# Performance work log

Hardware: AMD Instinct MI355X
Metric: run time of the kernel (lower is better)

## Reference

```python
import jax, jax.numpy as jnp
import numpy as np
import math

D_MODEL = 1024
N_HEADS = 16
D_K = D_MODEL // N_HEADS


def setup_inputs() -> dict:
    key = jax.random.key(0)
    ks = jax.random.split(key, 9)
    B, N = 2, 8192
    s = 1.0 / math.sqrt(D_MODEL)
    x = jax.random.normal(ks[0], (B, N, D_MODEL), dtype=jnp.float32)
    Wq = jax.random.normal(ks[1], (D_MODEL, D_MODEL), dtype=jnp.float32) * s
    bq = jnp.zeros((D_MODEL,), dtype=jnp.float32)
    Wk = jax.random.normal(ks[2], (D_MODEL, D_MODEL), dtype=jnp.float32) * s
    bk = jnp.zeros((D_MODEL,), dtype=jnp.float32)
    Wv = jax.random.normal(ks[3], (D_MODEL, D_MODEL), dtype=jnp.float32) * s
    bv = jnp.zeros((D_MODEL,), dtype=jnp.float32)
    Wo = jax.random.normal(ks[4], (D_MODEL, D_MODEL), dtype=jnp.float32) * s
    bo = jnp.zeros((D_MODEL,), dtype=jnp.float32)
    return {"x": x, "Wq": Wq, "bq": bq, "Wk": Wk, "bk": bk,
            "Wv": Wv, "bv": bv, "Wo": Wo, "bo": bo}


def _fft_circulant_attention(Q, K, V):
    # Q,K,V: (B,H,N,d_k); FFT along the sequence axis (axis=2)
    B, H, N, d_k = Q.shape
    scale = 1.0 / math.sqrt(d_k)
    Q_fft = jnp.fft.rfft(Q, axis=2)
    K_fft = jnp.fft.rfft(K, axis=2)
    # circular cross-correlation summed over d_k -> (B,H,Nf)
    scores_fft = jnp.sum(Q_fft * jnp.conj(K_fft), axis=-1)
    scores = jnp.fft.irfft(scores_fft, n=N, axis=2) * scale  # (B,H,N)
    attn = jax.nn.softmax(scores, axis=-1)                    # (B,H,N)
    attn_fft = jnp.fft.rfft(attn, axis=2)                     # (B,H,Nf)
    V_fft = jnp.fft.rfft(V, axis=2)                           # (B,H,Nf,d_k)
    out_fft = attn_fft[..., None] * V_fft
    return jnp.fft.irfft(out_fft, n=N, axis=2)                # (B,H,N,d_k)


def reference(x, Wq, bq, Wk, bk, Wv, bv, Wo, bo):
    B, N, _ = x.shape
    # torch Linear: x @ W.T + b
    def proj(W, b):
        return (x @ W.T + b).reshape(B, N, N_HEADS, D_K).transpose(0, 2, 1, 3)
    Q = proj(Wq, bq)
    K = proj(Wk, bk)
    V = proj(Wv, bv)
    O = _fft_circulant_attention(Q, K, V)          # (B,H,N,d_k)
    O = O.transpose(0, 2, 1, 3).reshape(B, N, D_MODEL)
    return O @ Wo.T + bo
```

## Files before the change

kernel.cpp:

```cpp
#include <hip/hip_runtime.h>
#include <math.h>
#include <stdint.h>

#define NDIM 8192
#define DM 1024
#define NH 16
#define DKH 64
#define BATCH 2
#define NSPLIT 16
#define NTF 256
#define NPTF (NDIM / NTF)

typedef __attribute__((ext_vector_type(8))) short short8v;
typedef __attribute__((ext_vector_type(4))) float f32x4;

__device__ inline float bf2f(unsigned short u) {
  return __uint_as_float(((unsigned int)u) << 16);
}
__device__ inline unsigned short f2bf(float f) {
  unsigned int u = __float_as_uint(f);
  u += 0x7fffu + ((u >> 16) & 1u);
  return (unsigned short)(u >> 16);
}
__device__ inline float2 cmul(float2 a, float2 b) {
  return make_float2(a.x * b.x - a.y * b.y, a.x * b.y + a.y * b.x);
}
__device__ inline float2 cmulc(float2 a, float2 b) {
  return make_float2(a.x * b.x + a.y * b.y, a.y * b.x - a.x * b.y);
}

__device__ inline void gload_lds16(const void* g, void* l) {
  __builtin_amdgcn_global_load_lds(
      (const __attribute__((address_space(1))) unsigned int*)(uintptr_t)g,
      (__attribute__((address_space(3))) unsigned int*)(uintptr_t)l, 16, 0, 0);
}

__global__ void twiddle_init(float2* tw) {
  int k = blockIdx.x * blockDim.x + threadIdx.x;
  if (k < NDIM) {
    double a = -2.0 * 3.14159265358979323846 * (double)k / (double)NDIM;
    tw[k] = make_float2((float)cos(a), (float)sin(a));
  }
}

__global__ __launch_bounds__(256)
void split_x(const float* __restrict__ x, unsigned short* __restrict__ xhi,
             unsigned short* __restrict__ xlo) {
  size_t i = ((size_t)blockIdx.x * 256 + threadIdx.x) * 4;
  float4 v = *(const float4*)&x[i];
  ushort4 h, l;
  h.x = f2bf(v.x); l.x = f2bf(v.x - bf2f(h.x));
  h.y = f2bf(v.y); l.y = f2bf(v.y - bf2f(h.y));
  h.z = f2bf(v.z); l.z = f2bf(v.z - bf2f(h.z));
  h.w = f2bf(v.w); l.w = f2bf(v.w - bf2f(h.w));
  *(ushort4*)&xhi[i] = h;
  *(ushort4*)&xlo[i] = l;
}

__global__ __launch_bounds__(256)
void split_w(const float* __restrict__ Wq, const float* __restrict__ Wk,
             const float* __restrict__ Wv, const float* __restrict__ Wo,
             unsigned short* __restrict__ whi, unsigned short* __restrict__ wlo,
             unsigned short* __restrict__ wob) {
  int z = blockIdx.z;
  const float* W = (z == 0) ? Wq : ((z == 1) ? Wk : ((z == 2) ? Wv : Wo));
  size_t i = ((size_t)blockIdx.x * 256 + threadIdx.x) * 4;
  float4 v = *(const float4*)&W[i];
  ushort4 h, l;
  h.x = f2bf(v.x); l.x = f2bf(v.x - bf2f(h.x));
  h.y = f2bf(v.y); l.y = f2bf(v.y - bf2f(h.y));
  h.z = f2bf(v.z); l.z = f2bf(v.z - bf2f(h.z));
  h.w = f2bf(v.w); l.w = f2bf(v.w - bf2f(h.w));
  if (z < 3) {
    *(ushort4*)&whi[(size_t)z * DM * DM + i] = h;
    *(ushort4*)&wlo[(size_t)z * DM * DM + i] = l;
  } else {
    *(ushort4*)&wob[i] = h;
  }
}

__device__ inline void fft_fwd(float2* __restrict__ s, const float2* __restrict__ tw, int tid) {
  const float C = 0.70710678118654752f;
  for (int lm = 10; lm >= 1; lm -= 3) {
    int m = 1 << lm;
    int sh = 10 - lm;
    __syncthreads();
    for (int t = tid; t < NDIM / 8; t += NTF) {
      int p = t & (m - 1);
      int i0 = ((t >> lm) << (lm + 3)) + p;
      float2 x0 = s[i0],       x1 = s[i0 + m],     x2 = s[i0 + 2 * m], x3 = s[i0 + 3 * m];
      float2 x4 = s[i0 + 4 * m], x5 = s[i0 + 5 * m], x6 = s[i0 + 6 * m], x7 = s[i0 + 7 * m];
      float2 e0 = {x0.x + x4.x, x0.y + x4.y}, o0 = {x0.x - x4.x, x0.y - x4.y};
      float2 e1 = {x1.x + x5.x, x1.y + x5.y}, o1 = {x1.x - x5.x, x1.y - x5.y};
      float2 e2 = {x2.x + x6.x, x2.y + x6.y}, o2 = {x2.x - x6.x, x2.y - x6.y};
      float2 e3 = {x3.x + x7.x, x3.y + x7.y}, o3 = {x3.x - x7.x, x3.y - x7.y};
      float2 t1 = {C * (o1.x + o1.y), C * (o1.y - o1.x)};
      float2 t2 = {o2.y, -o2.x};
      float2 t3 = {C * (o3.y - o3.x), -C * (o3.x + o3.y)};
      float2 pe = {e0.x + e2.x, e0.y + e2.y}, qe = {e0.x - e2.x, e0.y - e2.y};
      float2 re = {e1.x + e3.x, e1.y + e3.y}, se = {e1.x - e3.x, e1.y - e3.y};
      float2 po = {o0.x + t2.x, o0.y + t2.y}, qo = {o0.x - t2.x, o0.y - t2.y};
      float2 ro = {t1.x + t3.x, t1.y + t3.y}, so = {t1.x - t3.x, t1.y - t3.y};
      float2 y0 = {pe.x + re.x, pe.y + re.y};
      float2 y4 = {pe.x - re.x, pe.y - re.y};
      float2 y2 = {qe.x + se.y, qe.y - se.x};
      float2 y6 = {qe.x - se.y, qe.y + se.x};
      float2 y1 = {po.x + ro.x, po.y + ro.y};
      float2 y5 = {po.x - ro.x, po.y - ro.y};
      float2 y3 = {qo.x + so.y, qo.y - so.x};
      float2 y7 = {qo.x - so.y, qo.y + so.x};
      int e = p << sh;
      s[i0]         = y0;
      s[i0 + m]     = cmul(y1, tw[e]);
      s[i0 + 2 * m] = cmul(y2, tw[2 * e]);
      s[i0 + 3 * m] = cmul(y3, tw[3 * e]);
      s[i0 + 4 * m] = cmul(y4, tw[4 * e]);
      s[i0 + 5 * m] = cmul(y5, tw[5 * e]);
      s[i0 + 6 * m] = cmul(y6, tw[6 * e]);
      s[i0 + 7 * m] = cmul(y7, tw[7 * e]);
    }
  }
  __syncthreads();
  for (int t = tid; t < NDIM / 2; t += NTF) {
    int i0 = t * 2;
    float2 u = s[i0], v = s[i0 + 1];
    s[i0]     = make_float2(u.x + v.x, u.y + v.y);
    s[i0 + 1] = make_float2(u.x - v.x, u.y - v.y);
  }
  __syncthreads();
}

__device__ inline void fft_inv(float2* __restrict__ s, const float2* __restrict__ tw, int tid) {
  const float C = 0.70710678118654752f;
  __syncthreads();
  for (int t = tid; t < NDIM / 2; t += NTF) {
    int i0 = t * 2;
    float2 u = s[i0], v = s[i0 + 1];
    s[i0]     = make_float2(u.x + v.x, u.y + v.y);
    s[i0 + 1] = make_float2(u.x - v.x, u.y - v.y);
  }
  for (int lm = 1; lm <= 10; lm += 3) {
    int m = 1 << lm;
    int sh = 10 - lm;
    __syncthreads();
    for (int t = tid; t < NDIM / 8; t += NTF) {
      int p = t & (m - 1);
      int i0 = ((t >> lm) << (lm + 3)) + p;
      int e = p << sh;
      float2 z0 = s[i0];
      float2 z1 = cmulc(s[i0 + m],     tw[e]);
      float2 z2 = cmulc(s[i0 + 2 * m], tw[2 * e]);
      float2 z3 = cmulc(s[i0 + 3 * m], tw[3 * e]);
      float2 z4 = cmulc(s[i0 + 4 * m], tw[4 * e]);
      float2 z5 = cmulc(s[i0 + 5 * m], tw[5 * e]);
      float2 z6 = cmulc(s[i0 + 6 * m], tw[6 * e]);
      float2 z7 = cmulc(s[i0 + 7 * m], tw[7 * e]);
      float2 E0 = {z0.x + z4.x, z0.y + z4.y}, O0 = {z0.x - z4.x, z0.y - z4.y};
      float2 E1 = {z1.x + z5.x, z1.y + z5.y}, O1 = {z1.x - z5.x, z1.y - z5.y};
      float2 E2 = {z2.x + z6.x, z2.y + z6.y}, O2 = {z2.x - z6.x, z2.y - z6.y};
      float2 E3 = {z3.x + z7.x, z3.y + z7.y}, O3 = {z3.x - z7.x, z3.y - z7.y};
      float2 T1 = {C * (O1.x - O1.y), C * (O1.x + O1.y)};
      float2 T2 = {-O2.y, O2.x};
      float2 T3 = {-C * (O3.x + O3.y), C * (O3.x - O3.y)};
      float2 PE = {E0.x + E2.x, E0.y + E2.y}, QE = {E0.x - E2.x, E0.y - E2.y};
      float2 RE = {E1.x + E3.x, E1.y + E3.y}, SE = {E1.x - E3.x, E1.y - E3.y};
      float2 PO = {O0.x + T2.x, O0.y + T2.y}, QO = {O0.x - T2.x, O0.y - T2.y};
      float2 RO = {T1.x + T3.x, T1.y + T3.y}, SO = {T1.x - T3.x, T1.y - T3.y};
      s[i0]         = make_float2(PE.x + RE.x, PE.y + RE.y);
      s[i0 + 4 * m] = make_float2(PE.x - RE.x, PE.y - RE.y);
      s[i0 + 2 * m] = make_float2(QE.x - SE.y, QE.y + SE.x);
      s[i0 + 6 * m] = make_float2(QE.x + SE.y, QE.y - SE.x);
      s[i0 + m]     = make_float2(PO.x + RO.x, PO.y + RO.y);
      s[i0 + 5 * m] = make_float2(PO.x - RO.x, PO.y - RO.y);
      s[i0 + 3 * m] = make_float2(QO.x - SO.y, QO.y + SO.x);
      s[i0 + 7 * m] = make_float2(QO.x + SO.y, QO.y - SO.x);
    }
  }
  __syncthreads();
}

__device__ inline float blk_max(float v, float* red, int tid) {
  #pragma unroll
  for (int o = 32; o > 0; o >>= 1) v = fmaxf(v, __shfl_down(v, o, 64));
  __syncthreads();
  if ((tid & 63) == 0) red[tid >> 6] = v;
  __syncthreads();
  float r = fmaxf(fmaxf(red[0], red[1]), fmaxf(red[2], red[3]));
  __syncthreads();
  return r;
}
__device__ inline float blk_sum(float v, float* red, int tid) {
  #pragma unroll
  for (int o = 32; o > 0; o >>= 1) v += __shfl_down(v, o, 64);
  __syncthreads();
  if ((tid & 63) == 0) red[tid >> 6] = v;
  __syncthreads();
  float r = (red[0] + red[1]) + (red[2] + red[3]);
  __syncthreads();
  return r;
}

__global__ __launch_bounds__(512, 4)
void proj_gemm_mfma(const unsigned short* __restrict__ xhi, const unsigned short* __restrict__ xlo,
                    const unsigned short* __restrict__ whi, const unsigned short* __restrict__ wlo,
                    const float* __restrict__ bq, const float* __restrict__ bk,
                    const float* __restrict__ bv,
                    float* __restrict__ Qt, float* __restrict__ Kt, unsigned short* __restrict__ Vt) {
  int raw = blockIdx.x;
  int swz = (raw & 7) * 384 + (raw >> 3);
  int nb = (swz & 63) * 128;
  int cb = ((swz >> 6) & 7) * 128;
  int z  = swz >> 9;
  int b = z / 3, wsel = z % 3;
  bool full = (wsel < 2);
  const unsigned short* Wh = whi + (size_t)wsel * DM * DM;
  const unsigned short* Wl = wlo + (size_t)wsel * DM * DM;
  const float* bias = (wsel == 0) ? bq : ((wsel == 1) ? bk : bv);
  __shared__ unsigned short lAh[128 * 64], lAl[128 * 64];
  __shared__ unsigned short lBh[128 * 64], lBl[128 * 64];
  int tid = threadIdx.x;
  int lane = tid & 63, wid = tid >> 6;
  int wr = wid >> 2, wc = wid & 3;
  int srow = tid >> 3, sg = tid & 7;
  const unsigned short* gAh = Wh + (size_t)cb * DM;
  const unsigned short* gAl = Wl + (size_t)cb * DM;
  const unsigned short* gBh = xhi + ((size_t)b * NDIM + nb) * DM;
  const unsigned short* gBl = xlo + ((size_t)b * NDIM + nb) * DM;

  f32x4 acc[4][2];
  #pragma unroll
  for (int i = 0; i < 4; ++i)
    #pragma unroll
    for (int j = 0; j < 2; ++j) acc[i][j] = (f32x4){0.f, 0.f, 0.f, 0.f};

  int col = lane & 15, kg = lane >> 4;
  for (int k0 = 0; k0 < DM; k0 += 64) {
    #pragma unroll
    for (int i = 0; i < 2; ++i) {
      int r = i * 64 + srow;
      int gc = (sg ^ (r & 7)) * 8;
      size_t go = (size_t)r * DM + k0 + gc;
      int lo_ = r * 64 + sg * 8;
      gload_lds16(gAh + go, &lAh[lo_]);
      gload_lds16(gBh + go, &lBh[lo_]);
      if (full) {
        gload_lds16(gAl + go, &lAl[lo_]);
        gload_lds16(gBl + go, &lBl[lo_]);
      }
    }
    asm volatile("s_waitcnt vmcnt(0)");
    __syncthreads();
    #pragma unroll
    for (int kk = 0; kk < 2; ++kk) {
      short8v ah[4], al[4], bh_[2], bl_[2];
      #pragma unroll
      for (int mi = 0; mi < 4; ++mi) {
        int r = wr * 64 + mi * 16 + col;
        int s = r * 64 + (((kk * 4 + kg) ^ (r & 7)) * 8);
        ah[mi] = *(const short8v*)&lAh[s];
        if (full) al[mi] = *(const short8v*)&lAl[s];
      }
      #pragma unroll
      for (int ni = 0; ni < 2; ++ni) {
        int r = wc * 32 + ni * 16 + col;
        int s = r * 64 + (((kk * 4 + kg) ^ (r & 7)) * 8);
        bh_[ni] = *(const short8v*)&lBh[s];
        if (full) bl_[ni] = *(const short8v*)&lBl[s];
      }
      #pragma unroll
      for (int mi = 0; mi < 4; ++mi)
        #pragma unroll
        for (int ni = 0; ni < 2; ++ni) {
          acc[mi][ni] = __builtin_amdgcn_mfma_f32_16x16x32_bf16(ah[mi], bh_[ni], acc[mi][ni], 0, 0, 0);
          if (full) {
            acc[mi][ni] = __builtin_amdgcn_mfma_f32_16x16x32_bf16(ah[mi], bl_[ni], acc[mi][ni], 0, 0, 0);
            acc[mi][ni] = __builtin_amdgcn_mfma_f32_16x16x32_bf16(al[mi], bh_[ni], acc[mi][ni], 0, 0, 0);
          }
        }
    }
    __syncthreads();
  }
  size_t obase = (size_t)b * DM * NDIM;
  #pragma unroll
  for (int mi = 0; mi < 4; ++mi) {
    #pragma unroll
    for (int reg = 0; reg < 4; ++reg) {
      int c = cb + wr * 64 + mi * 16 + kg * 4 + reg;
      float bsv = bias[c];
      #pragma unroll
      for (int ni = 0; ni < 2; ++ni) {
        int n = nb + wc * 32 + ni * 16 + col;
        float v = acc[mi][ni][reg] + bsv;
        if (wsel < 2) {
          float* out = ((wsel == 0) ? Qt : Kt) + obase;
          out[(size_t)c * NDIM + n] = v;
        } else {
          Vt[obase + (size_t)c * NDIM + n] = f2bf(v);
        }
      }
    }
  }
}

__global__ __launch_bounds__(256)
void score_fft_kernel(const float* __restrict__ Qt, const float* __restrict__ Kt,
                      const float2* __restrict__ tw, float2* __restrict__ part) {
  extern __shared__ float2 buf[];
  int bh = blockIdx.x / NSPLIT;
  int split = blockIdx.x % NSPLIT;
  int b = bh / NH, h = bh % NH;
  int tid = threadIdx.x;
  float qfx[NPTF], qfy[NPTF], accx[NPTF], accy[NPTF];
  #pragma unroll
  for (int i = 0; i < NPTF; ++i) { accx[i] = 0.f; accy[i] = 0.f; }

  for (int dp = 0; dp < 2; ++dp) {
    int c0 = h * DKH + (split * 2 + dp) * 2;
    const float* q0 = Qt + ((size_t)b * DM + c0) * NDIM;
    const float* q1 = q0 + NDIM;
    const float* k0c = Kt + ((size_t)b * DM + c0) * NDIM;
    const float* k1c = k0c + NDIM;
    #pragma unroll
    for (int i = 0; i < NPTF; ++i) {
      int ii = i * NTF + tid;
      buf[ii] = make_float2(q0[ii], q1[ii]);
    }
    fft_fwd(buf, tw, tid);
    #pragma unroll
    for (int i = 0; i < NPTF; ++i) { float2 v = buf[i * NTF + tid]; qfx[i] = v.x; qfy[i] = v.y; }
    #pragma unroll
    for (int i = 0; i < NPTF; ++i) {
      int ii = i * NTF + tid;
      buf[ii] = make_float2(k0c[ii], k1c[ii]);
    }
    fft_fwd(buf, tw, tid);
    #pragma unroll
    for (int i = 0; i < NPTF; ++i) {
      float2 kf = buf[i * NTF + tid];
      accx[i] += qfx[i] * kf.x + qfy[i] * kf.y;
      accy[i] += qfy[i] * kf.x - qfx[i] * kf.y;
    }
  }
  float2* dst = part + ((size_t)bh * NSPLIT + split) * NDIM;
  #pragma unroll
  for (int i = 0; i < NPTF; ++i) dst[i * NTF + tid] = make_float2(accx[i], accy[i]);
}

__global__ __launch_bounds__(256)
void reduce_part(const float2* __restrict__ part, float2* __restrict__ sred) {
  #pragma unroll
  for (int rep = 0; rep < 2; ++rep) {
    size_t g = (size_t)blockIdx.x * 512 + rep * 256 + threadIdx.x;
    int bh = (int)(g >> 13);
    int i  = (int)(g & (NDIM - 1));
    float sx = 0.f, sy = 0.f;
    #pragma unroll
    for (int s = 0; s < NSPLIT; ++s) {
      float2 v = part[((size_t)bh * NSPLIT + s) * NDIM + i];
      sx += v.x; sy += v.y;
    }
    sred[g] = make_float2(sx, sy);
  }
}

__global__ __launch_bounds__(256)
void softmax_attn_kernel(const float2* __restrict__ sred, const float2* __restrict__ tw,
                         float2* __restrict__ attnf) {
  extern __shared__ float2 buf[];
  int bh = blockIdx.x;
  int tid = threadIdx.x;
  for (int i = tid; i < NDIM; i += NTF) buf[i] = sred[(size_t)bh * NDIM + i];
  fft_inv(buf, tw, tid);
  const float scale = 0.125f / (float)NDIM;
  float vals[NPTF];
  float lmax = -3.0e38f;
  #pragma unroll
  for (int i = 0; i < NPTF; ++i) {
    float v = buf[i * NTF + tid].x * scale;
    vals[i] = v;
    lmax = fmaxf(lmax, v);
  }
  float* red = (float*)buf;
  float gmax = blk_max(lmax, red, tid);
  float lsum = 0.f;
  #pragma unroll
  for (int i = 0; i < NPTF; ++i) { float e = expf(vals[i] - gmax); vals[i] = e; lsum += e; }
  float gsum = blk_sum(lsum, red, tid);
  float inv = 1.0f / gsum;
  #pragma unroll
  for (int i = 0; i < NPTF; ++i) buf[i * NTF + tid] = make_float2(vals[i] * inv, 0.f);
  fft_fwd(buf, tw, tid);
  for (int i = tid; i < NDIM; i += NTF) attnf[(size_t)bh * NDIM + i] = buf[i];
}

__global__ __launch_bounds__(256)
void out_fft_kernel(const unsigned short* __restrict__ Vt, const float2* __restrict__ attnf,
                    const float2* __restrict__ tw, unsigned short* __restrict__ Ot) {
  extern __shared__ float2 buf[];
  int idx = blockIdx.x;
  int b = idx / (DM / 2), cp = idx % (DM / 2);
  int c0 = cp * 2;
  int h = c0 >> 6;
  int bh = b * NH + h;
  int tid = threadIdx.x;
  const unsigned short* v0 = Vt + ((size_t)b * DM + c0) * NDIM;
  const unsigned short* v1 = v0 + NDIM;
  for (int i = tid; i < NDIM; i += NTF) buf[i] = make_float2(bf2f(v0[i]), bf2f(v1[i]));
  fft_fwd(buf, tw, tid);
  for (int i = tid; i < NDIM; i += NTF) {
    float2 vf = buf[i];
    float2 af = attnf[(size_t)bh * NDIM + i];
    buf[i] = cmul(vf, af);
  }
  fft_inv(buf, tw, tid);
  const float invn = 1.0f / (float)NDIM;
  unsigned short* o0 = Ot + ((size_t)b * DM + c0) * NDIM;
  unsigned short* o1 = o0 + NDIM;
  for (int i = tid; i < NDIM; i += NTF) {
    float2 v = buf[i];
    o0[i] = f2bf(v.x * invn);
    o1[i] = f2bf(v.y * invn);
  }
}

__global__ __launch_bounds__(256)
void transpose_ot(const unsigned short* __restrict__ Ot, unsigned short* __restrict__ Ont) {
  int b = blockIdx.z;
  int cb = blockIdx.y * 64, n0 = blockIdx.x * 64;
  __shared__ unsigned short t[64][68];
  int tid = threadIdx.x;
  int r = tid >> 4, c4 = (tid & 15) * 4;
  const unsigned short* src = Ot + (size_t)b * DM * NDIM;
  #pragma unroll
  for (int i = 0; i < 4; ++i) {
    ushort4 v = *(const ushort4*)&src[(size_t)(cb + i * 16 + r) * NDIM + n0 + c4];
    *(ushort4*)&t[i * 16 + r][c4] = v;
  }
  __syncthreads();
  unsigned short* dst = Ont + (size_t)b * NDIM * DM;
  #pragma unroll
  for (int i = 0; i < 4; ++i) {
    int n = i * 16 + r;
    ushort4 v;
    v.x = t[c4 + 0][n]; v.y = t[c4 + 1][n]; v.z = t[c4 + 2][n]; v.w = t[c4 + 3][n];
    *(ushort4*)&dst[(size_t)(n0 + n) * DM + cb + c4] = v;
  }
}

__global__ __launch_bounds__(512, 4)
void final_gemm_mfma(const unsigned short* __restrict__ Ont, const unsigned short* __restrict__ Wob,
                     const float* __restrict__ bo, float* __restrict__ out) {
  int raw = blockIdx.x;
  int swz = (raw & 7) * 128 + (raw >> 3);
  int nb = (swz & 63) * 128;
  int pb = ((swz >> 6) & 7) * 128;
  int b  = swz >> 9;
  __shared__ unsigned short lA[128 * 64], lB[128 * 64];
  int tid = threadIdx.x;
  int lane = tid & 63, wid = tid >> 6;
  int wr = wid >> 2, wc = wid & 3;
  int srow = tid >> 3, sg = tid & 7;
  const unsigned short* gA = Ont + ((size_t)b * NDIM + nb) * DM;
  const unsigned short* gB = Wob + (size_t)pb * DM;

  f32x4 acc[4][2];
  #pragma unroll
  for (int i = 0; i < 4; ++i)
    #pragma unroll
    for (int j = 0; j < 2; ++j) acc[i][j] = (f32x4){0.f, 0.f, 0.f, 0.f};

  int col = lane & 15, kg = lane >> 4;
  for (int k0 = 0; k0 < DM; k0 += 64) {
    #pragma unroll
    for (int i = 0; i < 2; ++i) {
      int r = i * 64 + srow;
      int gc = (sg ^ (r & 7)) * 8;
      size_t go = (size_t)r * DM + k0 + gc;
      int lo_ = r * 64 + sg * 8;
      gload_lds16(gA + go, &lA[lo_]);
      gload_lds16(gB + go, &lB[lo_]);
    }
    asm volatile("s_waitcnt vmcnt(0)");
    __syncthreads();
    #pragma unroll
    for (int kk = 0; kk < 2; ++kk) {
      short8v af[4], bf[2];
      #pragma unroll
      for (int mi = 0; mi < 4; ++mi) {
        int r = wr * 64 + mi * 16 + col;
        af[mi] = *(const short8v*)&lA[r * 64 + (((kk * 4 + kg) ^ (r & 7)) * 8)];
      }
      #pragma unroll
      for (int ni = 0; ni < 2; ++ni) {
        int r = wc * 32 + ni * 16 + col;
        bf[ni] = *(const short8v*)&lB[r * 64 + (((kk * 4 + kg) ^ (r & 7)) * 8)];
      }
      #pragma unroll
      for (int mi = 0; mi < 4; ++mi)
        #pragma unroll
        for (int ni = 0; ni < 2; ++ni)
          acc[mi][ni] = __builtin_amdgcn_mfma_f32_16x16x32_bf16(af[mi], bf[ni], acc[mi][ni], 0, 0, 0);
    }
    __syncthreads();
  }
  #pragma unroll
  for (int mi = 0; mi < 4; ++mi) {
    #pragma unroll
    for (int reg = 0; reg < 4; ++reg) {
      int n = nb + wr * 64 + mi * 16 + kg * 4 + reg;
      size_t rowoff = ((size_t)b * NDIM + n) * DM;
      #pragma unroll
      for (int ni = 0; ni < 2; ++ni) {
        int cp = pb + wc * 32 + ni * 16 + col;
        out[rowoff + cp] = acc[mi][ni][reg] + bo[cp];
      }
    }
  }
}

extern "C" void kernel_launch(void* const* d_in, const int* in_sizes, int n_in,
                              void* d_out, int out_size, void* d_ws, size_t ws_size,
                              hipStream_t stream) {
  (void)in_sizes; (void)n_in; (void)out_size;
  const float* x  = (const float*)d_in[0];
  const float* Wq = (const float*)d_in[1]; const float* bq = (const float*)d_in[2];
  const float* Wk = (const float*)d_in[3]; const float* bk = (const float*)d_in[4];
  const float* Wv = (const float*)d_in[5]; const float* bv = (const float*)d_in[6];
  const float* Wo = (const float*)d_in[7]; const float* bo = (const float*)d_in[8];

  char* ws = (char*)d_ws;
  size_t off = 0;
  float2* tw = (float2*)(ws + off); off += (size_t)NDIM * sizeof(float2);
  float*  Qt = (float*)(ws + off);  off += (size_t)BATCH * DM * NDIM * 4;
  float*  Kt = (float*)(ws + off);  off += (size_t)BATCH * DM * NDIM * 4;
  unsigned short* Vt  = (unsigned short*)(ws + off); off += (size_t)BATCH * DM * NDIM * 2;
  size_t xhi_off = off;
  unsigned short* Xhi = (unsigned short*)(ws + off); off += (size_t)BATCH * NDIM * DM * 2;
  size_t xlo_off = off;
  unsigned short* Xlo = (unsigned short*)(ws + off); off += (size_t)BATCH * NDIM * DM * 2;
  unsigned short* Whi = (unsigned short*)(ws + off); off += (size_t)3 * DM * DM * 2;
  unsigned short* Wlo = (unsigned short*)(ws + off); off += (size_t)3 * DM * DM * 2;
  unsigned short* Wob = (unsigned short*)(ws + off); off += (size_t)DM * DM * 2;
  float2* part  = (float2*)(ws + xhi_off);
  float2* attnf = (float2*)(ws + xlo_off);
  float2* sred  = (float2*)(ws + xlo_off + 4194304);
  unsigned short* Ot  = (unsigned short*)Qt;
  unsigned short* Ont = (unsigned short*)Kt;

  if (ws_size < off) return;

  twiddle_init<<<32, 256, 0, stream>>>(tw);
  split_x<<<(BATCH * NDIM * DM) / (256 * 4), 256, 0, stream>>>(x, Xhi, Xlo);
  split_w<<<dim3((DM * DM) / (256 * 4), 1, 4), 256, 0, stream>>>(Wq, Wk, Wv, Wo, Whi, Wlo, Wob);

  proj_gemm_mfma<<<3072, 512, 0, stream>>>(Xhi, Xlo, Whi, Wlo, bq, bk, bv, Qt, Kt, Vt);

  score_fft_kernel<<<BATCH * NH * NSPLIT, NTF, NDIM * sizeof(float2), stream>>>(Qt, Kt, tw, part);
  reduce_part<<<(BATCH * NH * NDIM) / 512, 256, 0, stream>>>(part, sred);
  softmax_attn_kernel<<<BATCH * NH, NTF, NDIM * sizeof(float2), stream>>>(sred, tw, attnf);
  out_fft_kernel<<<BATCH * DM / 2, NTF, NDIM * sizeof(float2), stream>>>(Vt, attnf, tw, Ot);

  transpose_ot<<<dim3(NDIM / 64, DM / 64, BATCH), 256, 0, stream>>>(Ot, Ont);
  final_gemm_mfma<<<1024, 512, 0, stream>>>(Ont, Wob, bo, (float*)d_out);
}
```

Before: 571.3 us.

## Halve projection GEMM K-tile, raise occupancy bound, drop block swizzle

The projection GEMM now stages 32-wide K slices instead of 64, which halves its LDS footprint (from 64KB to 32KB) and changes the XOR swizzle to match the new row width. Both GEMMs raise the launch-bounds occupancy hint from 4 to 8 blocks per SM and replace the 1D swizzled block mapping with a plain 3D grid. The aim is more resident waves to hide load latency. The cost is twice as many barrier/wait iterations per K, a tighter register budget, and possibly worse L2 locality without the swizzle.

Measured after the change: 1.958 ms. 3.43x slower.

```diff
diff --git a/kernel.cpp b/kernel.cpp
--- a/kernel.cpp
+++ b/kernel.cpp
@@ -200,28 +200,26 @@
   return r;
 }
 
-__global__ __launch_bounds__(512, 4)
+__global__ __launch_bounds__(512, 8)
 void proj_gemm_mfma(const unsigned short* __restrict__ xhi, const unsigned short* __restrict__ xlo,
                     const unsigned short* __restrict__ whi, const unsigned short* __restrict__ wlo,
                     const float* __restrict__ bq, const float* __restrict__ bk,
                     const float* __restrict__ bv,
                     float* __restrict__ Qt, float* __restrict__ Kt, unsigned short* __restrict__ Vt) {
-  int raw = blockIdx.x;
-  int swz = (raw & 7) * 384 + (raw >> 3);
-  int nb = (swz & 63) * 128;
-  int cb = ((swz >> 6) & 7) * 128;
-  int z  = swz >> 9;
+  int z = blockIdx.z;
   int b = z / 3, wsel = z % 3;
   bool full = (wsel < 2);
   const unsigned short* Wh = whi + (size_t)wsel * DM * DM;
   const unsigned short* Wl = wlo + (size_t)wsel * DM * DM;
   const float* bias = (wsel == 0) ? bq : ((wsel == 1) ? bk : bv);
-  __shared__ unsigned short lAh[128 * 64], lAl[128 * 64];
-  __shared__ unsigned short lBh[128 * 64], lBl[128 * 64];
+  int cb = blockIdx.y * 128;
+  int nb = blockIdx.x * 128;
+  __shared__ unsigned short lAh[128 * 32], lAl[128 * 32];
+  __shared__ unsigned short lBh[128 * 32], lBl[128 * 32];
   int tid = threadIdx.x;
   int lane = tid & 63, wid = tid >> 6;
   int wr = wid >> 2, wc = wid & 3;
-  int srow = tid >> 3, sg = tid & 7;
+  int srow = tid >> 2, sg = tid & 3;
   const unsigned short* gAh = Wh + (size_t)cb * DM;
   const unsigned short* gAl = Wl + (size_t)cb * DM;
   const unsigned short* gBh = xhi + ((size_t)b * NDIM + nb) * DM;
@@ -234,13 +232,12 @@
     for (int j = 0; j < 2; ++j) acc[i][j] = (f32x4){0.f, 0.f, 0.f, 0.f};
 
   int col = lane & 15, kg = lane >> 4;
-  for (int k0 = 0; k0 < DM; k0 += 64) {
-    #pragma unroll
-    for (int i = 0; i < 2; ++i) {
-      int r = i * 64 + srow;
-      int gc = (sg ^ (r & 7)) * 8;
-      size_t go = (size_t)r * DM + k0 + gc;
-      int lo_ = r * 64 + sg * 8;
+  int ssig = (srow >> 1) & 3;
+  for (int k0 = 0; k0 < DM; k0 += 32) {
+    {
+      int gc = (sg ^ ssig) * 8;
+      size_t go = (size_t)srow * DM + k0 + gc;
+      int lo_ = srow * 32 + sg * 8;
       gload_lds16(gAh + go, &lAh[lo_]);
       gload_lds16(gBh + go, &lBh[lo_]);
       if (full) {
@@ -250,20 +247,19 @@
     }
     asm volatile("s_waitcnt vmcnt(0)");
     __syncthreads();
-    #pragma unroll
-    for (int kk = 0; kk < 2; ++kk) {
+    {
       short8v ah[4], al[4], bh_[2], bl_[2];
       #pragma unroll
       for (int mi = 0; mi < 4; ++mi) {
         int r = wr * 64 + mi * 16 + col;
-        int s = r * 64 + (((kk * 4 + kg) ^ (r & 7)) * 8);
+        int s = r * 32 + ((kg ^ ((r >> 1) & 3)) * 8);
         ah[mi] = *(const short8v*)&lAh[s];
         if (full) al[mi] = *(const short8v*)&lAl[s];
       }
       #pragma unroll
       for (int ni = 0; ni < 2; ++ni) {
         int r = wc * 32 + ni * 16 + col;
-        int s = r * 64 + (((kk * 4 + kg) ^ (r & 7)) * 8);
+        int s = r * 32 + ((kg ^ ((r >> 1) & 3)) * 8);
         bh_[ni] = *(const short8v*)&lBh[s];
         if (full) bl_[ni] = *(const short8v*)&lBl[s];
       }
@@ -447,14 +443,12 @@
   }
 }
 
-__global__ __launch_bounds__(512, 4)
+__global__ __launch_bounds__(512, 8)
 void final_gemm_mfma(const unsigned short* __restrict__ Ont, const unsigned short* __restrict__ Wob,
                      const float* __restrict__ bo, float* __restrict__ out) {
-  int raw = blockIdx.x;
-  int swz = (raw & 7) * 128 + (raw >> 3);
-  int nb = (swz & 63) * 128;
-  int pb = ((swz >> 6) & 7) * 128;
-  int b  = swz >> 9;
+  int b = blockIdx.z;
+  int nb = blockIdx.x * 128;
+  int pb = blockIdx.y * 128;
   __shared__ unsigned short lA[128 * 64], lB[128 * 64];
   int tid = threadIdx.x;
   int lane = tid & 63, wid = tid >> 6;
@@ -553,7 +547,8 @@
   split_x<<<(BATCH * NDIM * DM) / (256 * 4), 256, 0, stream>>>(x, Xhi, Xlo);
   split_w<<<dim3((DM * DM) / (256 * 4), 1, 4), 256, 0, stream>>>(Wq, Wk, Wv, Wo, Whi, Wlo, Wob);
 
-  proj_gemm_mfma<<<3072, 512, 0, stream>>>(Xhi, Xlo, Whi, Wlo, bq, bk, bv, Qt, Kt, Vt);
+  dim3 pg(NDIM / 128, DM / 128, 3 * BATCH);
+  proj_gemm_mfma<<<pg, 512, 0, stream>>>(Xhi, Xlo, Whi, Wlo, bq, bk, bv, Qt, Kt, Vt);
 
   score_fft_kernel<<<BATCH * NH * NSPLIT, NTF, NDIM * sizeof(float2), stream>>>(Qt, Kt, tw, part);
   reduce_part<<<(BATCH * NH * NDIM) / 512, 256, 0, stream>>>(part, sred);
@@ -561,5 +556,5 @@
   out_fft_kernel<<<BATCH * DM / 2, NTF, NDIM * sizeof(float2), stream>>>(Vt, attnf, tw, Ot);
 
   transpose_ot<<<dim3(NDIM / 64, DM / 64, BATCH), 256, 0, stream>>>(Ot, Ont);
-  final_gemm_mfma<<<1024, 512, 0, stream>>>(Ont, Wob, bo, (float*)d_out);
-}
+  final_gemm_mfma<<<dim3(NDIM / 128, DM / 128, BATCH), 512, 0, stream>>>(Ont, Wob, bo, (float*)d_out);
+}
```
